# Performance work log

Measured on AMD Instinct MI355X. Metric: run time of the kernel, lower is better.

The kernel has to match this reference:

```python
import jax, jax.numpy as jnp
import numpy as np

SLOPE = 25.0   # surrogate.fast_sigmoid(slope=25)
THRESH = 1.0   # snntorch default threshold
BN_EPS = 1e-5
LN_EPS = 1e-5

@jax.custom_vjp
def spike(x):
    return (x > 0).astype(x.dtype)

def _spike_fwd(x):
    return (x > 0).astype(x.dtype), x

def _spike_bwd(x, g):
    # fast_sigmoid surrogate gradient: 1 / (slope*|x| + 1)^2
    return (g / (SLOPE * jnp.abs(x) + 1.0) ** 2,)

spike.defvjp(_spike_fwd, _spike_bwd)

def lif(inp, mem, beta):
    # snntorch Leaky (reset_mechanism='subtract'):
    # reset from previous mem, then integrate, then fire
    reset = spike(mem - THRESH)
    mem = beta * mem + inp - reset * THRESH
    spk = spike(mem - THRESH)
    return spk, mem

def _forward(L_norm, X_seq, conv_w, conv_b, bn_gamma, bn_beta, bn_mean, bn_var,
             gcn1_w, gcn1_b, mask1, gcn2_w, gcn2_b, mask2, beta2,
             attn_w1, attn_b1, attn_w2, attn_b2,
             cls_w1, cls_b1, ln_gamma, ln_beta, cls_w2, cls_b2):
    B = X_seq.shape[0]
    N = L_norm.shape[1]            # 64 nodes
    # [B,T,N,1] -> [B,N,T]
    x = jnp.squeeze(X_seq, -1).transpose(0, 2, 1)
    # causal conv1d (pad left k-1=2) + inference BatchNorm1d
    y = jax.lax.conv_general_dilated(x, conv_w, (1,), [(2, 0)],
                                     dimension_numbers=('NCH', 'OIH', 'NCH'))
    y = y + conv_b[None, :, None]
    y = (y - bn_mean[None, :, None]) * (bn_gamma[None, :, None]
        * jax.lax.rsqrt(bn_var[None, :, None] + BN_EPS)) + bn_beta[None, :, None]
    # dynamic Laplacian masks (constant across steps -> hoisted out of scan)
    m1 = jax.nn.sigmoid(mask1 + mask1.T) * 0.5
    m2 = jax.nn.sigmoid(mask2 + mask2.T) * 0.5
    L1 = L_norm * m1[None]         # [B,N,N]
    L2 = L_norm * m2[None]
    xs = y.transpose(2, 0, 1)[..., None]   # [T,B,N,1]

    def step(carry, xt):
        mem_t, mem_g1, mem_g2 = carry
        spk_t, mem_t = lif(xt, mem_t, 0.9)
        cur1 = jnp.einsum('bij,bjf->bif', L1, spk_t @ gcn1_w) + gcn1_b
        spk1, mem_g1 = lif(cur1, mem_g1, 0.85)
        cur2 = jnp.einsum('bij,bjf->bif', L2, spk1 @ gcn2_w) + gcn2_b
        spk2, mem_g2 = lif(cur2, mem_g2, beta2)
        return (mem_t, mem_g1, mem_g2), mem_g2.reshape(B, -1)

    init = (jnp.zeros((B, N, 1), x.dtype),
            jnp.zeros((B, N, 16), x.dtype),
            jnp.zeros((B, N, 32), x.dtype))
    _, pots = jax.lax.scan(step, init, xs)       # [T,B,N*32]
    pots = pots.transpose(1, 0, 2)               # [B,T,2048]
    # temporal attention decoder
    scores = jnp.tanh(pots @ attn_w1 + attn_b1) @ attn_w2 + attn_b2  # [B,T,1]
    w = jax.nn.softmax(scores, axis=1)
    ctx = jnp.sum(pots * w, axis=1)              # [B,2048]
    h = ctx @ cls_w1 + cls_b1                    # [B,128]
    mu = jnp.mean(h, axis=-1, keepdims=True)
    var = jnp.var(h, axis=-1, keepdims=True)
    h = (h - mu) * jax.lax.rsqrt(var + LN_EPS) * ln_gamma + ln_beta
    h = jax.nn.gelu(h, approximate=False)        # dropout is identity at eval
    return h @ cls_w2 + cls_b2                   # [B,4]

def setup_inputs() -> dict:
    key = jax.random.key(0)
    ks = jax.random.split(key, 16)
    B, T, N = 4096, 15, 64
    f32 = jnp.float32
    def xavier(k, shape):
        lim = float(np.sqrt(6.0 / (shape[0] + shape[1])))
        return jax.random.uniform(k, shape, f32, -lim, lim)
    return {
        'L_norm': jax.random.normal(ks[0], (B, N, N), f32),
        'X_seq': jax.random.normal(ks[1], (B, T, N, 1), f32),
        'conv_w': jax.random.normal(ks[2], (64, 64, 3), f32) / np.sqrt(64 * 3),
        'conv_b': jnp.zeros((64,), f32),
        'bn_gamma': jnp.ones((64,), f32),
        'bn_beta': jnp.zeros((64,), f32),
        'bn_mean': jnp.zeros((64,), f32),
        'bn_var': jnp.ones((64,), f32),
        'gcn1_w': xavier(ks[3], (1, 16)),
        'gcn1_b': jnp.zeros((16,), f32),
        'mask1': jnp.ones((N, N), f32),
        'gcn2_w': xavier(ks[4], (16, 32)),
        'gcn2_b': jnp.zeros((32,), f32),
        'mask2': jnp.ones((N, N), f32),
        'beta2': jnp.asarray(0.9, f32),
        'attn_w1': xavier(ks[5], (2048, 32)),
        'attn_b1': jnp.zeros((32,), f32),
        'attn_w2': xavier(ks[6], (32, 1)),
        'attn_b2': jnp.zeros((1,), f32),
        'cls_w1': xavier(ks[7], (2048, 128)),
        'cls_b1': jnp.zeros((128,), f32),
        'ln_gamma': jnp.ones((128,), f32),
        'ln_beta': jnp.zeros((128,), f32),
        'cls_w2': xavier(ks[8], (128, 4)),
        'cls_b2': jnp.zeros((4,), f32),
    }

def reference(L_norm, X_seq, conv_w, conv_b, bn_gamma, bn_beta, bn_mean, bn_var,
              gcn1_w, gcn1_b, mask1, gcn2_w, gcn2_b, mask2, beta2,
              attn_w1, attn_b1, attn_w2, attn_b2,
              cls_w1, cls_b1, ln_gamma, ln_beta, cls_w2, cls_b2):
    return _forward(L_norm, X_seq, conv_w, conv_b, bn_gamma, bn_beta, bn_mean, bn_var,
                    gcn1_w, gcn1_b, mask1, gcn2_w, gcn2_b, mask2, beta2,
                    attn_w1, attn_b1, attn_w2, attn_b2,
                    cls_w1, cls_b1, ln_gamma, ln_beta, cls_w2, cls_b2)
```

## Files before the change

### kernel.cpp

```cpp
#include <hip/hip_runtime.h>
#include <math.h>

#define WS_M1_F    0
#define WS_M2_F    4096
#define WS_BNSC_F  8192
#define WS_BNSH_F  8256
#define WS_WT_F    8448
#define OFF_W1T    83968
#define OFF_CW1H   215040
#define OFF_CW1L   739328
#define OFF_XCUR   1263616
#define OFF_DYN    16992256
#define PER_BATCH_POTS_B 61440
#define PER_BATCH_CTX_B  8192

typedef _Float16 v8h __attribute__((ext_vector_type(8)));
typedef short v8s __attribute__((ext_vector_type(8)));
typedef float v4f __attribute__((ext_vector_type(4)));
typedef float v16f __attribute__((ext_vector_type(16)));

__device__ __forceinline__ unsigned short f2h_u(float x) {
  _Float16 h = (_Float16)x;
  union { _Float16 h; unsigned short u; } v; v.h = h; return v.u;
}
__device__ __forceinline__ unsigned short bf16t(float x) {
  union { float f; unsigned int u; } v; v.f = x; return (unsigned short)(v.u >> 16);
}
__device__ __forceinline__ float bf16tof(unsigned short s) {
  union { unsigned int u; float f; } v; v.u = ((unsigned int)s) << 16; return v.f;
}

__global__ __launch_bounds__(256) void k_prep(
    const float* __restrict__ mask1, const float* __restrict__ mask2,
    const float* __restrict__ conv_w, const float* __restrict__ conv_b,
    const float* __restrict__ bn_gamma, const float* __restrict__ bn_beta,
    const float* __restrict__ bn_mean, const float* __restrict__ bn_var,
    const float* __restrict__ attn_w1, const float* __restrict__ cls_w1,
    float* __restrict__ wsf, unsigned short* __restrict__ w1t,
    unsigned short* __restrict__ cw1h, unsigned short* __restrict__ cw1l)
{
  const int gid = blockIdx.x * 256 + threadIdx.x;
  const int gsz = gridDim.x * 256;
  float* m1 = wsf + WS_M1_F;
  float* m2 = wsf + WS_M2_F;
  float* bnsc = wsf + WS_BNSC_F;
  float* bnsh = wsf + WS_BNSH_F;
  float* wT = wsf + WS_WT_F;
  for (int e = gid; e < 4096; e += gsz) {
    int i = e >> 6, j = e & 63;
    float s1 = mask1[e] + mask1[j * 64 + i];
    float s2 = mask2[e] + mask2[j * 64 + i];
    m1[e] = 0.5f / (1.f + expf(-s1));
    m2[e] = 0.5f / (1.f + expf(-s2));
  }
  for (int e = gid; e < 64; e += gsz) {
    float sc = bn_gamma[e] * rsqrtf(bn_var[e] + 1e-5f);
    bnsc[e] = sc;
    bnsh[e] = (conv_b[e] - bn_mean[e]) * sc + bn_beta[e];
  }
  for (int e = gid; e < 12288; e += gsz) {
    int o = e / 192, ik = e % 192;
    wT[ik * 64 + o] = conv_w[e];
  }
  for (int e = gid; e < 65536; e += gsz) {
    int n = e >> 11, i = e & 2047;
    w1t[e] = f2h_u(attn_w1[i * 32 + n]);
  }
  for (int e = gid; e < 262144; e += gsz) {
    int n = e >> 11, k = e & 2047;
    float x = cls_w1[k * 128 + n];
    unsigned short h = bf16t(x);
    cw1h[e] = h;
    cw1l[e] = bf16t(x - bf16tof(h));
  }
}

__global__ __launch_bounds__(256) void k_conv(
    const float* __restrict__ X_seq, const float* __restrict__ wsf,
    float* __restrict__ xcur_g)
{
  __shared__ float xraw[960];
  const int tid = threadIdx.x;
  const int lane = tid & 63;
  const int wv = tid >> 6;
  const int b = blockIdx.x;
  const float* bnsc = wsf + WS_BNSC_F;
  const float* bnsh = wsf + WS_BNSH_F;
  const float* wT = wsf + WS_WT_F;
  for (int e = tid; e < 960; e += 256) xraw[e] = X_seq[(size_t)b * 960 + e];
  __syncthreads();
  const int o = lane;
  const int t0 = wv, t1 = wv + 4, t2 = wv + 8, t3 = wv + 12;
  float a0 = 0.f, a1 = 0.f, a2 = 0.f, a3 = 0.f;
  for (int i = 0; i < 64; ++i) {
    const float w0 = wT[(3 * i + 0) * 64 + o];
    const float w1 = wT[(3 * i + 1) * 64 + o];
    const float w2 = wT[(3 * i + 2) * 64 + o];
    float xa = (t0 >= 2) ? xraw[(t0 - 2) * 64 + i] : 0.f;
    float xb = (t0 >= 1) ? xraw[(t0 - 1) * 64 + i] : 0.f;
    a0 += w0 * xa + w1 * xb + w2 * xraw[t0 * 64 + i];
    a1 += w0 * xraw[(t1 - 2) * 64 + i] + w1 * xraw[(t1 - 1) * 64 + i] + w2 * xraw[t1 * 64 + i];
    a2 += w0 * xraw[(t2 - 2) * 64 + i] + w1 * xraw[(t2 - 1) * 64 + i] + w2 * xraw[t2 * 64 + i];
    if (t3 < 15)
      a3 += w0 * xraw[(t3 - 2) * 64 + i] + w1 * xraw[(t3 - 1) * 64 + i] + w2 * xraw[t3 * 64 + i];
  }
  const float sc = bnsc[o], sh = bnsh[o];
  float* xg = xcur_g + (size_t)b * 960;
  xg[t0 * 64 + o] = a0 * sc + sh;
  xg[t1 * 64 + o] = a1 * sc + sh;
  xg[t2 * 64 + o] = a2 * sc + sh;
  if (t3 < 15) xg[t3 * 64 + o] = a3 * sc + sh;
}

__global__ __launch_bounds__(256) void k_main(
    const float* __restrict__ L_norm, const float* __restrict__ xcur_g,
    const float* __restrict__ gcn1_w, const float* __restrict__ gcn1_b,
    const float* __restrict__ gcn2_w, const float* __restrict__ gcn2_b,
    const float* __restrict__ beta2p,
    const float* __restrict__ wsf, unsigned short* __restrict__ pots,
    int b0)
{
  __shared__ float xcur[960];
  __shared__ float zp[2 * 64];
  __shared__ __align__(16) unsigned short spk1T[16 * 72];
  __shared__ __align__(16) float Z2f[64 * 20];

  const int tid = threadIdx.x;
  const int lane = tid & 63;
  const int wv = tid >> 6;
  const int b = b0 + blockIdx.x;

  const float* m1 = wsf + WS_M1_F;
  const float* m2 = wsf + WS_M2_F;

  for (int e = tid; e < 960; e += 256) xcur[e] = xcur_g[(size_t)b * 960 + e];

  float L1h[32];
  const int kb1 = (wv & 1) * 32;
  if (wv >= 2) {
    const float* Lb = L_norm + (size_t)b * 4096 + lane * 64 + kb1;
    const float* mr = m1 + lane * 64 + kb1;
#pragma unroll
    for (int q4 = 0; q4 < 8; ++q4) {
      float4 lv = *(const float4*)(Lb + 4 * q4);
      float4 mv = *(const float4*)(mr + 4 * q4);
      L1h[4 * q4 + 0] = lv.x * mv.x;
      L1h[4 * q4 + 1] = lv.y * mv.y;
      L1h[4 * q4 + 2] = lv.z * mv.z;
      L1h[4 * q4 + 3] = lv.w * mv.w;
    }
  }

  v8s A_hi[2], A_lo[2];
  {
    const int irow = wv * 16 + (lane & 15);
    const int quad = (lane >> 4) & 3;
#pragma unroll
    for (int kb = 0; kb < 2; ++kb) {
      const float* Lb = L_norm + (size_t)b * 4096 + irow * 64 + kb * 32 + quad * 8;
      const float* mr = m2 + irow * 64 + kb * 32 + quad * 8;
      float4 la = *(const float4*)Lb, lb2 = *(const float4*)(Lb + 4);
      float4 ma = *(const float4*)mr, mb = *(const float4*)(mr + 4);
      float v[8] = { la.x * ma.x, la.y * ma.y, la.z * ma.z, la.w * ma.w,
                     lb2.x * mb.x, lb2.y * mb.y, lb2.z * mb.z, lb2.w * mb.w };
#pragma unroll
      for (int e = 0; e < 8; ++e) {
        unsigned short h = bf16t(v[e]);
        unsigned short l = bf16t(v[e] - bf16tof(h));
        A_hi[kb][e] = (short)h;
        A_lo[kb][e] = (short)l;
      }
    }
  }

  v8s W_hi, W_lo;
  {
    const int n = lane & 31;
    const int kh = (lane >> 5) & 1;
#pragma unroll
    for (int e = 0; e < 8; ++e) {
      float x = gcn2_w[(kh * 8 + e) * 32 + n];
      unsigned short h = bf16t(x);
      unsigned short l = bf16t(x - bf16tof(h));
      W_hi[e] = (short)h;
      W_lo[e] = (short)l;
    }
  }

  const float b2h = gcn2_b[lane & 31];
  const int np = tid >> 3;
  const int cp = tid & 7;
  float w1c[2], b1c[2];
#pragma unroll
  for (int d = 0; d < 2; ++d) { w1c[d] = gcn1_w[2 * cp + d]; b1c[d] = gcn1_b[2 * cp + d]; }
  const float beta2 = beta2p[0];

  float mem_t = 0.f;
  float mg1[4] = {0.f, 0.f, 0.f, 0.f};
  v16f mg2;
#pragma unroll
  for (int r = 0; r < 16; ++r) mg2[r] = 0.f;

  unsigned short* pbase = pots + (size_t)blockIdx.x * 30720 + (lane & 31);

  auto stage_b = [&](int tm1) {
    const int m = lane & 31;
    const int half = lane >> 5;
    const float* zr = Z2f + (wv * 32 + m) * 20 + half * 8;
    float4 za = *(const float4*)zr;
    float4 zb = *(const float4*)(zr + 4);
    float vv[8] = {za.x, za.y, za.z, za.w, zb.x, zb.y, zb.z, zb.w};
    v8s Ah, Al;
#pragma unroll
    for (int e = 0; e < 8; ++e) {
      unsigned short h = bf16t(vv[e]);
      unsigned short l = bf16t(vv[e] - bf16tof(h));
      Ah[e] = (short)h;
      Al[e] = (short)l;
    }
    v16f acc;
#pragma unroll
    for (int r = 0; r < 16; ++r) {
      float rs = (mg2[r] > 1.f) ? 1.f : 0.f;
      acc[r] = fmaf(beta2, mg2[r], b2h - rs);
    }
    acc = __builtin_amdgcn_mfma_f32_32x32x16_bf16(Ah, W_hi, acc, 0, 0, 0);
    acc = __builtin_amdgcn_mfma_f32_32x32x16_bf16(Al, W_hi, acc, 0, 0, 0);
    acc = __builtin_amdgcn_mfma_f32_32x32x16_bf16(Ah, W_lo, acc, 0, 0, 0);
    mg2 = acc;
    unsigned short* pb = pbase + (size_t)tm1 * 2048;
#pragma unroll
    for (int r = 0; r < 16; ++r) {
      int i = wv * 32 + (r & 3) + 8 * (r >> 2) + 4 * half;
      pb[i * 32] = f2h_u(acc[r]);
    }
  };

  __syncthreads();

  for (int t = 0; t < 15; ++t) {
    if (wv >= 2) {
      float xc = xcur[t * 64 + lane];
      float rs = (mem_t > 1.f) ? 1.f : 0.f;
      mem_t = 0.9f * mem_t + xc - rs;
      float sp = (mem_t > 1.f) ? 1.f : 0.f;
      int spi = __float_as_int(sp);
      float zh = 0.f;
#pragma unroll
      for (int k = 0; k < 32; ++k) {
        float s = __int_as_float(__builtin_amdgcn_readlane(spi, kb1 + k));
        zh = fmaf(s, L1h[k], zh);
      }
      zp[(wv & 1) * 64 + lane] = zh;
    } else if (t > 0) {
      stage_b(t - 1);
    }
    __syncthreads();
    {
      float2 q0 = *(const float2*)&zp[2 * np];
      float2 q1 = *(const float2*)&zp[64 + 2 * np];
      float z0 = q0.x + q1.x;
      float z1v = q0.y + q1.y;
#pragma unroll
      for (int d = 0; d < 2; ++d) {
        float cur0 = fmaf(z0, w1c[d], b1c[d]);
        float rs0 = (mg1[d * 2 + 0] > 1.f) ? 1.f : 0.f;
        mg1[d * 2 + 0] = 0.85f * mg1[d * 2 + 0] + cur0 - rs0;
        unsigned int bits0 = (mg1[d * 2 + 0] > 1.f) ? 0x3F80u : 0u;
        float cur1 = fmaf(z1v, w1c[d], b1c[d]);
        float rs1 = (mg1[d * 2 + 1] > 1.f) ? 1.f : 0.f;
        mg1[d * 2 + 1] = 0.85f * mg1[d * 2 + 1] + cur1 - rs1;
        unsigned int bits1 = (mg1[d * 2 + 1] > 1.f) ? 0x3F80u : 0u;
        *(unsigned int*)&spk1T[(2 * cp + d) * 72 + 2 * np] = bits0 | (bits1 << 16);
      }
    }
    __syncthreads();
    {
      const int c = lane & 15;
      const int quad = (lane >> 4) & 3;
      const unsigned short* bp = spk1T + c * 72 + quad * 8;
      v8s B0 = *(const v8s*)(bp);
      v8s B1 = *(const v8s*)(bp + 32);
      v4f acc = {0.f, 0.f, 0.f, 0.f};
      acc = __builtin_amdgcn_mfma_f32_16x16x32_bf16(A_hi[0], B0, acc, 0, 0, 0);
      acc = __builtin_amdgcn_mfma_f32_16x16x32_bf16(A_lo[0], B0, acc, 0, 0, 0);
      acc = __builtin_amdgcn_mfma_f32_16x16x32_bf16(A_hi[1], B1, acc, 0, 0, 0);
      acc = __builtin_amdgcn_mfma_f32_16x16x32_bf16(A_lo[1], B1, acc, 0, 0, 0);
      const int r0 = wv * 16 + quad * 4;
#pragma unroll
      for (int r = 0; r < 4; ++r) Z2f[(r0 + r) * 20 + c] = acc[r];
    }
    __syncthreads();
  }
  if (wv < 2) stage_b(14);
}

__global__ __launch_bounds__(256) void k_att(
    const unsigned short* __restrict__ pots,
    const unsigned short* __restrict__ w1t,
    const float* __restrict__ attn_b1, const float* __restrict__ attn_w2,
    const float* __restrict__ attn_b2,
    unsigned short* __restrict__ ctxh, unsigned short* __restrict__ ctxl)
{
  __shared__ float sred[8 * 256];
  __shared__ __align__(16) float wbuf[4 * 16];
  const int tid = threadIdx.x;
  const int lane = tid & 63;
  const int wv = tid >> 6;
  const int m = lane & 15;
  const int quad = lane >> 4;
  const int koff = quad * 8;
  const unsigned short* pb = pots + (size_t)blockIdx.x * 30720;

  v4f a0 = {0.f, 0.f, 0.f, 0.f}, a1 = {0.f, 0.f, 0.f, 0.f};
  {
    const unsigned short* Ap = pb + (size_t)m * 2048 + koff;
    const unsigned short* B0p = w1t + (size_t)m * 2048 + koff;
    const unsigned short* B1p = w1t + (size_t)(m + 16) * 2048 + koff;
#pragma unroll 4
    for (int c = wv * 16; c < wv * 16 + 16; ++c) {
      v8h A = *(const v8h*)(Ap + c * 32);
      v8h B0 = *(const v8h*)(B0p + c * 32);
      v8h B1 = *(const v8h*)(B1p + c * 32);
      a0 = __builtin_amdgcn_mfma_f32_16x16x32_f16(A, B0, a0, 0, 0, 0);
      a1 = __builtin_amdgcn_mfma_f32_16x16x32_f16(A, B1, a1, 0, 0, 0);
    }
  }
#pragma unroll
  for (int j = 0; j < 4; ++j) {
    sred[j * 256 + tid] = a0[j];
    sred[(j + 4) * 256 + tid] = a1[j];
  }
  __syncthreads();
  float s0[4], s1[4];
#pragma unroll
  for (int j = 0; j < 4; ++j) {
    s0[j] = sred[j * 256 + 0 * 64 + lane] + sred[j * 256 + 1 * 64 + lane]
          + sred[j * 256 + 2 * 64 + lane] + sred[j * 256 + 3 * 64 + lane];
    s1[j] = sred[(j + 4) * 256 + 0 * 64 + lane] + sred[(j + 4) * 256 + 1 * 64 + lane]
          + sred[(j + 4) * 256 + 2 * 64 + lane] + sred[(j + 4) * 256 + 3 * 64 + lane];
  }
  float wlar[16];
  {
    const int n = m;
    const float b1a = attn_b1[n], b1b = attn_b1[n + 16];
    const float w2a = attn_w2[n], w2b = attn_w2[n + 16];
    const float b2 = attn_b2[0];
    float sc[4];
#pragma unroll
    for (int r = 0; r < 4; ++r) {
      float v = tanhf(s0[r] + b1a) * w2a + tanhf(s1[r] + b1b) * w2b;
      v += __shfl_xor(v, 1, 64);
      v += __shfl_xor(v, 2, 64);
      v += __shfl_xor(v, 4, 64);
      v += __shfl_xor(v, 8, 64);
      sc[r] = v + b2;
    }
    float mx = -1e30f;
#pragma unroll
    for (int r = 0; r < 4; ++r) if (quad * 4 + r < 15) mx = fmaxf(mx, sc[r]);
    mx = fmaxf(mx, __shfl_xor(mx, 16, 64));
    mx = fmaxf(mx, __shfl_xor(mx, 32, 64));
    float e[4], den = 0.f;
#pragma unroll
    for (int r = 0; r < 4; ++r) {
      e[r] = (quad * 4 + r < 15) ? expf(sc[r] - mx) : 0.f;
      den += e[r];
    }
    den += __shfl_xor(den, 16, 64);
    den += __shfl_xor(den, 32, 64);
    const float inv = 1.f / den;
    if ((lane & 15) == 0) {
      v4f wq = {e[0] * inv, e[1] * inv, e[2] * inv, e[3] * inv};
      *(v4f*)&wbuf[wv * 16 + quad * 4] = wq;
    }
#pragma unroll
    for (int q4 = 0; q4 < 4; ++q4) {
      float4 v = *(const float4*)&wbuf[wv * 16 + q4 * 4];
      wlar[q4 * 4 + 0] = v.x; wlar[q4 * 4 + 1] = v.y;
      wlar[q4 * 4 + 2] = v.z; wlar[q4 * 4 + 3] = v.w;
    }
  }
  float cv[8] = {0.f, 0.f, 0.f, 0.f, 0.f, 0.f, 0.f, 0.f};
  const unsigned short* pp = pb + tid * 8;
#pragma unroll
  for (int t = 0; t < 15; ++t) {
    v8h pv = *(const v8h*)(pp + (size_t)t * 2048);
    const float w = wlar[t];
#pragma unroll
    for (int j = 0; j < 8; ++j) cv[j] = fmaf(w, (float)pv[j], cv[j]);
  }
  unsigned short hv[8], lv[8];
#pragma unroll
  for (int j = 0; j < 8; ++j) {
    unsigned short h = bf16t(cv[j]);
    hv[j] = h;
    lv[j] = bf16t(cv[j] - bf16tof(h));
  }
  *(uint4*)(ctxh + (size_t)blockIdx.x * 2048 + tid * 8) = *(const uint4*)hv;
  *(uint4*)(ctxl + (size_t)blockIdx.x * 2048 + tid * 8) = *(const uint4*)lv;
}

__global__ __launch_bounds__(256) void k_cls(
    const unsigned short* __restrict__ ctxh, const unsigned short* __restrict__ ctxl,
    const unsigned short* __restrict__ cw1h, const unsigned short* __restrict__ cw1l,
    const float* __restrict__ cls_b1,
    const float* __restrict__ ln_g, const float* __restrict__ ln_b,
    const float* __restrict__ cls_w2, const float* __restrict__ cls_b2,
    float* __restrict__ out, int b0)
{
  __shared__ float hbuf[16 * 132];
  const int tid = threadIdx.x;
  const int lane = tid & 63;
  const int wv = tid >> 6;
  const int m = lane & 15;
  const int quad = lane >> 4;
  const int koff = quad * 8;
  const int r0l = blockIdx.x * 16;

  v4f a0 = {0.f, 0.f, 0.f, 0.f}, a1 = {0.f, 0.f, 0.f, 0.f};
  {
    const unsigned short* Ah = ctxh + (size_t)(r0l + m) * 2048;
    const unsigned short* Al = ctxl + (size_t)(r0l + m) * 2048;
    const int n0 = wv * 32 + m;
    const unsigned short* B0h = cw1h + (size_t)n0 * 2048;
    const unsigned short* B0l = cw1l + (size_t)n0 * 2048;
    const unsigned short* B1h = cw1h + (size_t)(n0 + 16) * 2048;
    const unsigned short* B1l = cw1l + (size_t)(n0 + 16) * 2048;
#pragma unroll 4
    for (int kc = 0; kc < 64; ++kc) {
      const int kb = kc * 32 + koff;
      v8s vAh = *(const v8s*)(Ah + kb);
      v8s vAl = *(const v8s*)(Al + kb);
      v8s vB0h = *(const v8s*)(B0h + kb);
      v8s vB0l = *(const v8s*)(B0l + kb);
      v8s vB1h = *(const v8s*)(B1h + kb);
      v8s vB1l = *(const v8s*)(B1l + kb);
      a0 = __builtin_amdgcn_mfma_f32_16x16x32_bf16(vAh, vB0h, a0, 0, 0, 0);
      a0 = __builtin_amdgcn_mfma_f32_16x16x32_bf16(vAl, vB0h, a0, 0, 0, 0);
      a0 = __builtin_amdgcn_mfma_f32_16x16x32_bf16(vAh, vB0l, a0, 0, 0, 0);
      a1 = __builtin_amdgcn_mfma_f32_16x16x32_bf16(vAh, vB1h, a1, 0, 0, 0);
      a1 = __builtin_amdgcn_mfma_f32_16x16x32_bf16(vAl, vB1h, a1, 0, 0, 0);
      a1 = __builtin_amdgcn_mfma_f32_16x16x32_bf16(vAh, vB1l, a1, 0, 0, 0);
    }
  }
  {
    const int n0 = wv * 32 + m;
    const float bb0 = cls_b1[n0], bb1 = cls_b1[n0 + 16];
#pragma unroll
    for (int r = 0; r < 4; ++r) {
      const int row = quad * 4 + r;
      hbuf[row * 132 + n0] = a0[r] + bb0;
      hbuf[row * 132 + n0 + 16] = a1[r] + bb1;
    }
  }
  __syncthreads();
  const float g0c = ln_g[lane], g1c = ln_g[lane + 64];
  const float b0c = ln_b[lane], b1c = ln_b[lane + 64];
  const float4 w2a = *(const float4*)(cls_w2 + lane * 4);
  const float4 w2b = *(const float4*)(cls_w2 + (lane + 64) * 4);
#pragma unroll
  for (int rr = 0; rr < 4; ++rr) {
    const int r = wv * 4 + rr;
    const float x0 = hbuf[r * 132 + lane];
    const float x1 = hbuf[r * 132 + 64 + lane];
    float s = x0 + x1, sq = x0 * x0 + x1 * x1;
#pragma unroll
    for (int mm = 32; mm >= 1; mm >>= 1) {
      s += __shfl_xor(s, mm, 64);
      sq += __shfl_xor(sq, mm, 64);
    }
    const float mu = s * (1.f / 128.f);
    const float var = sq * (1.f / 128.f) - mu * mu;
    const float rstd = rsqrtf(var + 1e-5f);
    float h0 = (x0 - mu) * rstd * g0c + b0c;
    float h1 = (x1 - mu) * rstd * g1c + b1c;
    h0 = 0.5f * h0 * (1.f + erff(h0 * 0.7071067811865475f));
    h1 = 0.5f * h1 * (1.f + erff(h1 * 0.7071067811865475f));
    float o0 = h0 * w2a.x + h1 * w2b.x;
    float o1 = h0 * w2a.y + h1 * w2b.y;
    float o2 = h0 * w2a.z + h1 * w2b.z;
    float o3 = h0 * w2a.w + h1 * w2b.w;
#pragma unroll
    for (int mm = 32; mm >= 1; mm >>= 1) {
      o0 += __shfl_xor(o0, mm, 64);
      o1 += __shfl_xor(o1, mm, 64);
      o2 += __shfl_xor(o2, mm, 64);
      o3 += __shfl_xor(o3, mm, 64);
    }
    if (lane == 0) {
      *(float4*)(out + (size_t)(b0 + r0l + r) * 4) =
          make_float4(o0 + cls_b2[0], o1 + cls_b2[1], o2 + cls_b2[2], o3 + cls_b2[3]);
    }
  }
}

extern "C" void kernel_launch(void* const* d_in, const int* in_sizes, int n_in,
                              void* d_out, int out_size, void* d_ws, size_t ws_size,
                              hipStream_t stream) {
  const float* L_norm   = (const float*)d_in[0];
  const float* X_seq    = (const float*)d_in[1];
  const float* conv_w   = (const float*)d_in[2];
  const float* conv_b   = (const float*)d_in[3];
  const float* bn_gamma = (const float*)d_in[4];
  const float* bn_beta  = (const float*)d_in[5];
  const float* bn_mean  = (const float*)d_in[6];
  const float* bn_var   = (const float*)d_in[7];
  const float* gcn1_w   = (const float*)d_in[8];
  const float* gcn1_b   = (const float*)d_in[9];
  const float* mask1    = (const float*)d_in[10];
  const float* gcn2_w   = (const float*)d_in[11];
  const float* gcn2_b   = (const float*)d_in[12];
  const float* mask2    = (const float*)d_in[13];
  const float* beta2    = (const float*)d_in[14];
  const float* attn_w1  = (const float*)d_in[15];
  const float* attn_b1  = (const float*)d_in[16];
  const float* attn_w2  = (const float*)d_in[17];
  const float* attn_b2  = (const float*)d_in[18];
  const float* cls_w1   = (const float*)d_in[19];
  const float* cls_b1   = (const float*)d_in[20];
  const float* ln_gamma = (const float*)d_in[21];
  const float* ln_beta  = (const float*)d_in[22];
  const float* cls_w2   = (const float*)d_in[23];
  const float* cls_b2   = (const float*)d_in[24];

  char* ws = (char*)d_ws;
  float* wsf = (float*)d_ws;
  unsigned short* w1t  = (unsigned short*)(ws + OFF_W1T);
  unsigned short* cw1h = (unsigned short*)(ws + OFF_CW1H);
  unsigned short* cw1l = (unsigned short*)(ws + OFF_CW1L);
  float* xcur_g = (float*)(ws + OFF_XCUR);

  long long avail = (long long)ws_size - (long long)OFF_DYN - 4096;
  long long per = PER_BATCH_POTS_B + PER_BATCH_CTX_B;
  int chunk = 4096;
  if (avail < per * 4096LL) {
    long long c = (avail > 0) ? (avail / per) : 64;
    if (c > 4096) c = 4096;
    c &= ~63LL;
    if (c < 64) c = 64;
    chunk = (int)c;
  }
  unsigned short* pots = (unsigned short*)(ws + OFF_DYN);
  unsigned short* ctxh = (unsigned short*)(ws + OFF_DYN + (size_t)chunk * PER_BATCH_POTS_B + 4096);
  unsigned short* ctxl = ctxh + (size_t)chunk * 2048;

  hipLaunchKernelGGL(k_prep, dim3(64), dim3(256), 0, stream,
                     mask1, mask2, conv_w, conv_b, bn_gamma, bn_beta, bn_mean, bn_var,
                     attn_w1, cls_w1, wsf, w1t, cw1h, cw1l);
  hipLaunchKernelGGL(k_conv, dim3(4096), dim3(256), 0, stream,
                     X_seq, wsf, xcur_g);

  for (int b0 = 0; b0 < 4096; b0 += chunk) {
    int cur = 4096 - b0;
    if (cur > chunk) cur = chunk;
    hipLaunchKernelGGL(k_main, dim3(cur), dim3(256), 0, stream,
                       L_norm, xcur_g, gcn1_w, gcn1_b, gcn2_w, gcn2_b, beta2,
                       wsf, pots, b0);
    hipLaunchKernelGGL(k_att, dim3(cur), dim3(256), 0, stream,
                       pots, w1t, attn_b1, attn_w2, attn_b2, ctxh, ctxl);
    hipLaunchKernelGGL(k_cls, dim3(cur / 16), dim3(256), 0, stream,
                       ctxh, ctxl, cw1h, cw1l, cls_b1, ln_gamma, ln_beta, cls_w2, cls_b2,
                       (float*)d_out, b0);
  }
}
```

Baseline: 597.2 us.

## Fuse conv, spiking GCN scan and attention pooling into one kernel with LDS potentials

Merges the causal conv+BN kernel, the LIF/GCN recurrence kernel and the attention-pooling kernel into a single per-batch kernel. The membrane potentials (15 timesteps x 2048 fp16) now stay in a 64KB shared-memory buffer with an XOR swizzle instead of going through global memory, and the conv output also stays in LDS. This removes about 60KB of global writes and reads per batch plus two launches. In exchange, LDS use per block rises to roughly 76KB, which limits occupancy, and the conv and attention phases now serialize inside one block.

```diff
diff --git a/kernel.cpp b/kernel.cpp
--- a/kernel.cpp
+++ b/kernel.cpp
@@ -9,10 +9,7 @@
 #define OFF_W1T    83968
 #define OFF_CW1H   215040
 #define OFF_CW1L   739328
-#define OFF_XCUR   1263616
-#define OFF_DYN    16992256
-#define PER_BATCH_POTS_B 61440
-#define PER_BATCH_CTX_B  8192
+#define OFF_CTX    1263616
 
 typedef _Float16 v8h __attribute__((ext_vector_type(8)));
 typedef short v8s __attribute__((ext_vector_type(8)));
@@ -75,55 +72,23 @@
   }
 }
 
-__global__ __launch_bounds__(256) void k_conv(
-    const float* __restrict__ X_seq, const float* __restrict__ wsf,
-    float* __restrict__ xcur_g)
-{
-  __shared__ float xraw[960];
-  const int tid = threadIdx.x;
-  const int lane = tid & 63;
-  const int wv = tid >> 6;
-  const int b = blockIdx.x;
-  const float* bnsc = wsf + WS_BNSC_F;
-  const float* bnsh = wsf + WS_BNSH_F;
-  const float* wT = wsf + WS_WT_F;
-  for (int e = tid; e < 960; e += 256) xraw[e] = X_seq[(size_t)b * 960 + e];
-  __syncthreads();
-  const int o = lane;
-  const int t0 = wv, t1 = wv + 4, t2 = wv + 8, t3 = wv + 12;
-  float a0 = 0.f, a1 = 0.f, a2 = 0.f, a3 = 0.f;
-  for (int i = 0; i < 64; ++i) {
-    const float w0 = wT[(3 * i + 0) * 64 + o];
-    const float w1 = wT[(3 * i + 1) * 64 + o];
-    const float w2 = wT[(3 * i + 2) * 64 + o];
-    float xa = (t0 >= 2) ? xraw[(t0 - 2) * 64 + i] : 0.f;
-    float xb = (t0 >= 1) ? xraw[(t0 - 1) * 64 + i] : 0.f;
-    a0 += w0 * xa + w1 * xb + w2 * xraw[t0 * 64 + i];
-    a1 += w0 * xraw[(t1 - 2) * 64 + i] + w1 * xraw[(t1 - 1) * 64 + i] + w2 * xraw[t1 * 64 + i];
-    a2 += w0 * xraw[(t2 - 2) * 64 + i] + w1 * xraw[(t2 - 1) * 64 + i] + w2 * xraw[t2 * 64 + i];
-    if (t3 < 15)
-      a3 += w0 * xraw[(t3 - 2) * 64 + i] + w1 * xraw[(t3 - 1) * 64 + i] + w2 * xraw[t3 * 64 + i];
-  }
-  const float sc = bnsc[o], sh = bnsh[o];
-  float* xg = xcur_g + (size_t)b * 960;
-  xg[t0 * 64 + o] = a0 * sc + sh;
-  xg[t1 * 64 + o] = a1 * sc + sh;
-  xg[t2 * 64 + o] = a2 * sc + sh;
-  if (t3 < 15) xg[t3 * 64 + o] = a3 * sc + sh;
-}
-
-__global__ __launch_bounds__(256) void k_main(
-    const float* __restrict__ L_norm, const float* __restrict__ xcur_g,
+__global__ __launch_bounds__(256) void k_fused(
+    const float* __restrict__ L_norm, const float* __restrict__ X_seq,
     const float* __restrict__ gcn1_w, const float* __restrict__ gcn1_b,
     const float* __restrict__ gcn2_w, const float* __restrict__ gcn2_b,
-    const float* __restrict__ beta2p,
-    const float* __restrict__ wsf, unsigned short* __restrict__ pots,
+    const float* __restrict__ beta2p, const float* __restrict__ wsf,
+    const unsigned short* __restrict__ w1t,
+    const float* __restrict__ attn_b1, const float* __restrict__ attn_w2,
+    const float* __restrict__ attn_b2,
+    unsigned short* __restrict__ ctxh, unsigned short* __restrict__ ctxl,
     int b0)
 {
-  __shared__ float xcur[960];
-  __shared__ float zp[2 * 64];
-  __shared__ __align__(16) unsigned short spk1T[16 * 72];
-  __shared__ __align__(16) float Z2f[64 * 20];
+  __shared__ __align__(16) unsigned short pots_s[16 * 2048];
+  __shared__ __align__(16) char smR[11776];
+  float* xcur = (float*)smR;
+  float* zp = (float*)(smR + 3840);
+  unsigned short* spk1T = (unsigned short*)(smR + 4352);
+  float* Z2f = (float*)(smR + 6656);
 
   const int tid = threadIdx.x;
   const int lane = tid & 63;
@@ -133,7 +98,36 @@
   const float* m1 = wsf + WS_M1_F;
   const float* m2 = wsf + WS_M2_F;
 
-  for (int e = tid; e < 960; e += 256) xcur[e] = xcur_g[(size_t)b * 960 + e];
+  {
+    float* xraw = (float*)pots_s;
+    for (int e = tid; e < 960; e += 256) xraw[e] = X_seq[(size_t)b * 960 + e];
+    *(uint4*)&pots_s[15 * 2048 + tid * 8] = make_uint4(0u, 0u, 0u, 0u);
+    __syncthreads();
+    const float* bnsc = wsf + WS_BNSC_F;
+    const float* bnsh = wsf + WS_BNSH_F;
+    const float* wT = wsf + WS_WT_F;
+    const int o = lane;
+    const int t0 = wv, t1 = wv + 4, t2 = wv + 8, t3 = wv + 12;
+    float a0 = 0.f, a1 = 0.f, a2 = 0.f, a3 = 0.f;
+    for (int i = 0; i < 64; ++i) {
+      const float w0 = wT[(3 * i + 0) * 64 + o];
+      const float w1 = wT[(3 * i + 1) * 64 + o];
+      const float w2 = wT[(3 * i + 2) * 64 + o];
+      float xa = (t0 >= 2) ? xraw[(t0 - 2) * 64 + i] : 0.f;
+      float xb = (t0 >= 1) ? xraw[(t0 - 1) * 64 + i] : 0.f;
+      a0 += w0 * xa + w1 * xb + w2 * xraw[t0 * 64 + i];
+      a1 += w0 * xraw[(t1 - 2) * 64 + i] + w1 * xraw[(t1 - 1) * 64 + i] + w2 * xraw[t1 * 64 + i];
+      a2 += w0 * xraw[(t2 - 2) * 64 + i] + w1 * xraw[(t2 - 1) * 64 + i] + w2 * xraw[t2 * 64 + i];
+      if (t3 < 15)
+        a3 += w0 * xraw[(t3 - 2) * 64 + i] + w1 * xraw[(t3 - 1) * 64 + i] + w2 * xraw[t3 * 64 + i];
+    }
+    const float sc = bnsc[o], sh = bnsh[o];
+    xcur[t0 * 64 + o] = a0 * sc + sh;
+    xcur[t1 * 64 + o] = a1 * sc + sh;
+    xcur[t2 * 64 + o] = a2 * sc + sh;
+    if (t3 < 15) xcur[t3 * 64 + o] = a3 * sc + sh;
+    __syncthreads();
+  }
 
   float L1h[32];
   const int kb1 = (wv & 1) * 32;
@@ -200,8 +194,6 @@
   v16f mg2;
 #pragma unroll
   for (int r = 0; r < 16; ++r) mg2[r] = 0.f;
-
-  unsigned short* pbase = pots + (size_t)blockIdx.x * 30720 + (lane & 31);
 
   auto stage_b = [&](int tm1) {
     const int m = lane & 31;
@@ -228,15 +220,14 @@
     acc = __builtin_amdgcn_mfma_f32_32x32x16_bf16(Al, W_hi, acc, 0, 0, 0);
     acc = __builtin_amdgcn_mfma_f32_32x32x16_bf16(Ah, W_lo, acc, 0, 0, 0);
     mg2 = acc;
-    unsigned short* pb = pbase + (size_t)tm1 * 2048;
+    const int xorv = (tm1 & 7) << 3;
+    const int base = tm1 * 2048 + m;
 #pragma unroll
     for (int r = 0; r < 16; ++r) {
       int i = wv * 32 + (r & 3) + 8 * (r >> 2) + 4 * half;
-      pb[i * 32] = f2h_u(acc[r]);
+      pots_s[(base + i * 32) ^ xorv] = f2h_u(acc[r]);
     }
   };
-
-  __syncthreads();
 
   for (int t = 0; t < 15; ++t) {
     if (wv >= 2) {
@@ -293,33 +284,23 @@
     __syncthreads();
   }
   if (wv < 2) stage_b(14);
-}
-
-__global__ __launch_bounds__(256) void k_att(
-    const unsigned short* __restrict__ pots,
-    const unsigned short* __restrict__ w1t,
-    const float* __restrict__ attn_b1, const float* __restrict__ attn_w2,
-    const float* __restrict__ attn_b2,
-    unsigned short* __restrict__ ctxh, unsigned short* __restrict__ ctxl)
-{
-  __shared__ float sred[8 * 256];
-  __shared__ __align__(16) float wbuf[4 * 16];
-  const int tid = threadIdx.x;
-  const int lane = tid & 63;
-  const int wv = tid >> 6;
+  __syncthreads();
+
+  float* sred = (float*)smR;
+  float* wbuf = (float*)(smR + 8192);
   const int m = lane & 15;
   const int quad = lane >> 4;
   const int koff = quad * 8;
-  const unsigned short* pb = pots + (size_t)blockIdx.x * 30720;
 
   v4f a0 = {0.f, 0.f, 0.f, 0.f}, a1 = {0.f, 0.f, 0.f, 0.f};
   {
-    const unsigned short* Ap = pb + (size_t)m * 2048 + koff;
+    const int axor = (m & 7) << 3;
+    const int abase = m * 2048 + koff;
     const unsigned short* B0p = w1t + (size_t)m * 2048 + koff;
     const unsigned short* B1p = w1t + (size_t)(m + 16) * 2048 + koff;
 #pragma unroll 4
     for (int c = wv * 16; c < wv * 16 + 16; ++c) {
-      v8h A = *(const v8h*)(Ap + c * 32);
+      v8h A = *(const v8h*)(pots_s + ((abase + c * 32) ^ axor));
       v8h B0 = *(const v8h*)(B0p + c * 32);
       v8h B1 = *(const v8h*)(B1p + c * 32);
       a0 = __builtin_amdgcn_mfma_f32_16x16x32_f16(A, B0, a0, 0, 0, 0);
@@ -382,10 +363,10 @@
     }
   }
   float cv[8] = {0.f, 0.f, 0.f, 0.f, 0.f, 0.f, 0.f, 0.f};
-  const unsigned short* pp = pb + tid * 8;
 #pragma unroll
   for (int t = 0; t < 15; ++t) {
-    v8h pv = *(const v8h*)(pp + (size_t)t * 2048);
+    const int idx = (t * 2048 + tid * 8) ^ ((t & 7) << 3);
+    v8h pv = *(const v8h*)(pots_s + idx);
     const float w = wlar[t];
 #pragma unroll
     for (int j = 0; j < 8; ++j) cv[j] = fmaf(w, (float)pv[j], cv[j]);
@@ -529,36 +510,29 @@
   unsigned short* w1t  = (unsigned short*)(ws + OFF_W1T);
   unsigned short* cw1h = (unsigned short*)(ws + OFF_CW1H);
   unsigned short* cw1l = (unsigned short*)(ws + OFF_CW1L);
-  float* xcur_g = (float*)(ws + OFF_XCUR);
-
-  long long avail = (long long)ws_size - (long long)OFF_DYN - 4096;
-  long long per = PER_BATCH_POTS_B + PER_BATCH_CTX_B;
+
+  long long avail = (long long)ws_size - (long long)OFF_CTX;
   int chunk = 4096;
-  if (avail < per * 4096LL) {
-    long long c = (avail > 0) ? (avail / per) : 64;
+  if (avail < 8192LL * 4096LL) {
+    long long c = (avail > 0) ? (avail / 8192) : 64;
     if (c > 4096) c = 4096;
     c &= ~63LL;
     if (c < 64) c = 64;
     chunk = (int)c;
   }
-  unsigned short* pots = (unsigned short*)(ws + OFF_DYN);
-  unsigned short* ctxh = (unsigned short*)(ws + OFF_DYN + (size_t)chunk * PER_BATCH_POTS_B + 4096);
+  unsigned short* ctxh = (unsigned short*)(ws + OFF_CTX);
   unsigned short* ctxl = ctxh + (size_t)chunk * 2048;
 
   hipLaunchKernelGGL(k_prep, dim3(64), dim3(256), 0, stream,
                      mask1, mask2, conv_w, conv_b, bn_gamma, bn_beta, bn_mean, bn_var,
                      attn_w1, cls_w1, wsf, w1t, cw1h, cw1l);
-  hipLaunchKernelGGL(k_conv, dim3(4096), dim3(256), 0, stream,
-                     X_seq, wsf, xcur_g);
 
   for (int b0 = 0; b0 < 4096; b0 += chunk) {
     int cur = 4096 - b0;
     if (cur > chunk) cur = chunk;
-    hipLaunchKernelGGL(k_main, dim3(cur), dim3(256), 0, stream,
-                       L_norm, xcur_g, gcn1_w, gcn1_b, gcn2_w, gcn2_b, beta2,
-                       wsf, pots, b0);
-    hipLaunchKernelGGL(k_att, dim3(cur), dim3(256), 0, stream,
-                       pots, w1t, attn_b1, attn_w2, attn_b2, ctxh, ctxl);
+    hipLaunchKernelGGL(k_fused, dim3(cur), dim3(256), 0, stream,
+                       L_norm, X_seq, gcn1_w, gcn1_b, gcn2_w, gcn2_b, beta2,
+                       wsf, w1t, attn_b1, attn_w2, attn_b2, ctxh, ctxl, b0);
     hipLaunchKernelGGL(k_cls, dim3(cur / 16), dim3(256), 0, stream,
                        ctxh, ctxl, cw1h, cw1l, cls_b1, ln_gamma, ln_beta, cls_w2, cls_b2,
                        (float*)d_out, b0);
```

After: 500.4 us. 16.2% less time.
